# Performance work log

Measured on AMD Instinct MI355X. Metric: run time of the kernel, lower is better.

## Reference

```python
import jax, jax.numpy as jnp
import numpy as np

DEPTH = 13                 # tree depth -> N = 2**DEPTH - 1 reaches (heap layout, outlet = node 0)
N = 2 ** DEPTH - 1         # 8191 reaches
T = 2048                   # timesteps


def setup_inputs() -> dict:
    key = jax.random.key(0)
    ks = jax.random.split(key, 8)
    u = lambda k, shape, lo, hi: jax.random.uniform(k, shape, minval=lo, maxval=hi, dtype=jnp.float32)
    return {
        "lateral_inflows": u(ks[0], (T, N), 0.0, 2.0),     # m^3/s lateral inflow per reach
        "manning_n":       u(ks[1], (N,), 0.025, 0.06),    # Manning roughness
        "lengths":         u(ks[2], (N,), 1000.0, 5000.0), # reach length [m]
        "slopes":          u(ks[3], (N,), 1e-4, 1e-2),     # bed slope (>= 1e-4 as in source)
        "width_coefs":     u(ks[4], (N,), 3.0, 10.0),      # w = wc * Q**we  (power-law geometry)
        "width_exps":      u(ks[5], (N,), 0.4, 0.6),
        "depth_coefs":     u(ks[6], (N,), 0.2, 0.5),       # h = dc * Q**de
        "depth_exps":      u(ks[7], (N,), 0.3, 0.45),
        "dt": 3600,                                        # routing timestep [s]
    }


def _mc_outflow(I_new, I_old, O_old, n, L, S, wc, we, dc, de, dt):
    """Variable-parameter Muskingum-Cunge update for one vector of reaches."""
    Qr = jnp.maximum(0.5 * (I_new + O_old), 1e-3)          # reference discharge
    h = dc * Qr ** de                                       # hydraulic depth
    w = wc * Qr ** we                                       # top width
    v = h ** (2.0 / 3.0) * jnp.sqrt(S) / n                  # Manning velocity
    c = jnp.maximum((5.0 / 3.0) * v, 1e-3)                  # kinematic celerity
    K = L / c                                               # travel time
    X = jnp.clip(0.5 * (1.0 - Qr / (w * S * c * L)), 0.0, 0.5)
    den = 2.0 * K * (1.0 - X) + dt
    C1 = (dt - 2.0 * K * X) / den
    C2 = (dt + 2.0 * K * X) / den
    C3 = (2.0 * K * (1.0 - X) - dt) / den
    return jnp.maximum(C1 * I_new + C2 * I_old + C3 * O_old, 0.0)


def reference(lateral_inflows, manning_n, lengths, slopes, width_coefs, width_exps,
              depth_coefs, depth_exps, dt):
    dtf = jnp.float32(dt)
    Np = lateral_inflows.shape[1]
    params = (manning_n, lengths, slopes, width_coefs, width_exps, depth_coefs, depth_exps)

    def step(carry, lat_t):
        I_old, O_old = carry                                # [N] prev inflow / outflow
        Q = jnp.zeros(Np, dtype=lat_t.dtype)                # new outflows this timestep
        I_all = jnp.zeros(Np, dtype=lat_t.dtype)
        # process levels leaves -> root (reverse topological order over the DAG)
        for l in range(DEPTH - 1, -1, -1):
            s, e = 2 ** l - 1, 2 ** (l + 1) - 1             # nodes of level l
            if l == DEPTH - 1:
                up = jnp.float32(0.0)                        # headwater reaches
            else:
                cs, ce = 2 ** (l + 1) - 1, 2 ** (l + 2) - 1  # children = level l+1
                up = Q[cs:ce:2] + Q[cs + 1:ce:2]             # sum of 2 upstream discharges
            I_new = lat_t[s:e] + up
            O_new = _mc_outflow(I_new, I_old[s:e], O_old[s:e],
                                *(p[s:e] for p in params), dtf)
            Q = Q.at[s:e].set(O_new)
            I_all = I_all.at[s:e].set(I_new)
        return (I_all, Q), Q[0]                              # outlet = root (index 0)

    init = (jnp.zeros(Np, jnp.float32), jnp.zeros(Np, jnp.float32))
    _, outlet_Q = jax.lax.scan(step, init, lateral_inflows)
    return outlet_Q                                          # [T]
```

## Files before the change

### kernel.cpp

```cpp
#include <hip/hip_runtime.h>


#define NN 8191
#define TT 2048
#define FBATCH 32
#define NBLK 39
#define BTHREADS 256

#define FLAGS_FOFF 16773120ull
#define REQ_BYTES  67106816ull
#define FLAG_STRIDE 16

#if __has_builtin(__builtin_amdgcn_exp2f)
__device__ __forceinline__ float fexp2(float x) { return __builtin_amdgcn_exp2f(x); }
#else
__device__ __forceinline__ float fexp2(float x) { return exp2f(x); }
#endif
#if __has_builtin(__builtin_amdgcn_logf)
__device__ __forceinline__ float flog2(float x) { return __builtin_amdgcn_logf(x); }
#else
__device__ __forceinline__ float flog2(float x) { return log2f(x); }
#endif
#if __has_builtin(__builtin_amdgcn_rcpf)
__device__ __forceinline__ float frcp(float x) { return __builtin_amdgcn_rcpf(x); }
#else
__device__ __forceinline__ float frcp(float x) { return 1.0f / x; }
#endif

__constant__ int g_level[NBLK] = {
    12,12,12,12,12,12,12,12,12,12,12,12,12,12,12,12,
    11,11,11,11,11,11,11,11,
    10,10,10,10,
    9,9,
    8,7,6,5,4,3,2,1,0};
__constant__ int g_cnt[NBLK] = {
    256,256,256,256,256,256,256,256,256,256,256,256,256,256,256,256,
    256,256,256,256,256,256,256,256,
    256,256,256,256,
    256,256,
    256,128,64,32,16,8,4,2,1};
__constant__ int g_first[13] = {38,37,36,35,34,33,32,31,30,28,24,16,0};
__constant__ unsigned long long g_off[13] = {
    16773120ull, 16769024ull, 16760832ull, 16744448ull, 16711680ull,
    16646144ull, 16515072ull, 16252928ull, 15728640ull, 14680064ull,
    12582912ull, 8388608ull, 0ull};

__device__ __forceinline__ void waitflags(const unsigned int* fa, const unsigned int* fb,
                                          unsigned int target)
{
    while (true) {
        unsigned int a = __hip_atomic_load(fa, __ATOMIC_RELAXED, __HIP_MEMORY_SCOPE_AGENT);
        unsigned int b = fb ? __hip_atomic_load(fb, __ATOMIC_RELAXED, __HIP_MEMORY_SCOPE_AGENT)
                            : a;
        if (a >= target && b >= target) break;
        __builtin_amdgcn_s_sleep(1);
    }
    __builtin_amdgcn_sched_barrier(0);
    asm volatile("" ::: "memory");
}

__global__ void zero_flags(unsigned int* flags)
{
    for (int i = threadIdx.x; i < NBLK * 4 * FLAG_STRIDE; i += 256) flags[i] = 0;
}

__global__ __launch_bounds__(BTHREADS, 1)
void pipe_kernel(const float* __restrict__ lat,
                 const float* __restrict__ nman,
                 const float* __restrict__ len,
                 const float* __restrict__ slp,
                 const float* __restrict__ wcf,
                 const float* __restrict__ wex,
                 const float* __restrict__ dcf,
                 const float* __restrict__ dex,
                 const int*   __restrict__ dtp,
                 float*       __restrict__ out,
                 float*       __restrict__ ws)
{
    const int bid = blockIdx.x;
    const int tid = threadIdx.x;
    const int lvl = g_level[bid];
    const int cnt = g_cnt[bid];
    const int W   = tid >> 6;
    const int wn  = cnt - W * 64;
    if (wn <= 0) return;

    const bool active = (tid < cnt);
    const int B = bid - g_first[lvl];
    const int m = B * 256 + (active ? tid : 0);
    const int node = ((1 << lvl) - 1) + m;
    const int wbase = B * 256 + W * 64;

    unsigned int* flags = (unsigned int*)(ws + FLAGS_FOFF);
    unsigned int* myflag = flags + ((size_t)bid * 4 + W) * FLAG_STRIDE;

    const bool haschild = (lvl < 12);
    const unsigned int* fa = nullptr;
    const unsigned int* fb = nullptr;
    if (haschild) {
        const int Fp = g_first[lvl + 1];
        const int nw = wn < 64 ? wn : 64;
        const int p0 = (2 * wbase) >> 6;
        const int p1 = (2 * wbase + 2 * nw - 1) >> 6;
        fa = flags + ((size_t)(Fp + (p0 >> 2)) * 4 + (p0 & 3)) * FLAG_STRIDE;
        fb = (p1 != p0)
           ? flags + ((size_t)(Fp + (p1 >> 2)) * 4 + (p1 & 3)) * FLAG_STRIDE
           : nullptr;
    }

    const int myW = 1 << lvl;
    const int childW = 1 << (lvl + 1);
    float* myBuf = ws + g_off[lvl];
    const unsigned long long* childBuf =
        haschild ? (const unsigned long long*)(ws + g_off[lvl + 1]) : nullptr;

    const float dtf = (float)dtp[0];

    float em, tkc, ex, k1;
    float Iold = 0.0f, Oold = 0.0f;
    {
        float n = nman[node], L = len[node], S = slp[node];
        float wc = wcf[node], we = wex[node], dc = dcf[node], de = dex[node];
        float dc23 = fexp2(0.6666667f * flog2(dc));
        float cc = 1.6666667f * dc23 * sqrtf(S) * frcp(n);
        float e23 = 0.6666667f * de;
        em  = -e23;
        tkc = 2.0f * L * frcp(cc);
        ex  = 1.0f - we - e23;
        k1  = 0.5f * frcp(S * L * wc * cc);
    }

    float laA[FBATCH], laB[FBATCH];
    unsigned long long cvA[FBATCH], cvB[FBATCH];

#define LATBURST(dst, tb)                                                      \
    if (active) {                                                              \
        _Pragma("unroll")                                                      \
        for (int k = 0; k < FBATCH; ++k) {                                     \
            const float* lp_ = lat + (size_t)((tb) + k) * NN + node;           \
            asm volatile("global_load_dword %0, %1, off"                       \
                         : "=v"(dst[k]) : "v"(lp_));                           \
        }                                                                      \
    }

#define CHILDBURST(dst, tb)                                                    \
    if (haschild && active) {                                                  \
        _Pragma("unroll")                                                      \
        for (int k = 0; k < FBATCH; ++k) {                                     \
            const unsigned long long* cp_ =                                    \
                childBuf + (((size_t)((tb) + k) * childW) >> 1) + m;           \
            asm volatile("global_load_dwordx2 %0, %1, off sc0 sc1"             \
                         : "=v"(dst[k]) : "v"(cp_));                           \
        }                                                                      \
    }

#define CHAIN(laC, cvC, tb)                                                    \
    if (active) {                                                              \
        _Pragma("unroll")                                                      \
        for (int k = 0; k < FBATCH; ++k) {                                     \
            float ch_ = 0.0f;                                                  \
            if (haschild) {                                                    \
                float c0_ = __uint_as_float((unsigned int)(cvC[k] & 0xffffffffull)); \
                float c1_ = __uint_as_float((unsigned int)(cvC[k] >> 32));     \
                ch_ = c0_ + c1_;                                               \
            }                                                                  \
            float Inew = laC[k] + ch_;                                         \
            float Qr = fmaxf(0.5f * (Inew + Oold), 1e-3f);                     \
            float lg = flog2(Qr);                                              \
            float twoK = tkc * fexp2(em * lg);                                 \
            float X = fmaxf(0.5f - k1 * fexp2(ex * lg), 0.0f);                 \
            float A = twoK * X;                                                \
            float Bv = twoK - A;                                               \
            float r = frcp(Bv + dtf);                                          \
            float num = dtf * (Inew + Iold - Oold) + A * (Iold - Inew) + Bv * Oold; \
            float O = fmaxf(num * r, 0.0f);                                    \
            Iold = Inew; Oold = O;                                             \
            if (lvl > 0)                                                       \
                __hip_atomic_store(myBuf + (size_t)((tb) + k) * myW + m, O,    \
                                   __ATOMIC_RELAXED, __HIP_MEMORY_SCOPE_AGENT);\
            else                                                               \
                out[(tb) + k] = O;                                             \
        }                                                                      \
    }

#define PHASE(laC, cvC, laN, cvN, T0)                                          \
    do {                                                                       \
        const int t1_ = (T0) + FBATCH;                                         \
        if (t1_ < TT) {                                                        \
            LATBURST(laN, t1_);                                                \
            if (haschild) waitflags(fa, fb, (unsigned int)(t1_ + FBATCH));     \
            CHILDBURST(cvN, t1_);                                              \
        }                                                                      \
        CHAIN(laC, cvC, (T0));                                                 \
        asm volatile("s_waitcnt vmcnt(0)" ::: "memory");                       \
        __builtin_amdgcn_sched_barrier(0);                                     \
        if (lvl > 0 && (tid & 63) == 0)                                        \
            __hip_atomic_store(myflag, (unsigned int)((T0) + FBATCH),          \
                               __ATOMIC_RELAXED, __HIP_MEMORY_SCOPE_AGENT);    \
    } while (0)

    LATBURST(laA, 0);
    if (haschild) waitflags(fa, fb, (unsigned int)FBATCH);
    CHILDBURST(cvA, 0);
    asm volatile("s_waitcnt vmcnt(0)" ::: "memory");
    __builtin_amdgcn_sched_barrier(0);

    for (int t0 = 0; t0 < TT; t0 += 2 * FBATCH) {
        PHASE(laA, cvA, laB, cvB, t0);
        PHASE(laB, cvB, laA, cvA, t0 + FBATCH);
    }
#undef LATBURST
#undef CHILDBURST
#undef CHAIN
#undef PHASE
}

#define NTHREADS 1024
__device__ __forceinline__ float mc_update_fb(float Inew, float Iold, float Oold,
                                              float em, float tkc, float ex, float k1,
                                              float dtf)
{
    float Qr = fmaxf(0.5f * (Inew + Oold), 1e-3f);
    float lg = flog2(Qr);
    float twoK = tkc * fexp2(em * lg);
    float X = fmaxf(0.5f - k1 * fexp2(ex * lg), 0.0f);
    float A = twoK * X;
    float B = twoK - A;
    float r = frcp(B + dtf);
    float C1 = (dtf - A) * r;
    float C2 = (dtf + A) * r;
    float C3 = (B - dtf) * r;
    return fmaxf(C1 * Inew + C2 * Iold + C3 * Oold, 0.0f);
}

__global__ __launch_bounds__(NTHREADS)
void route_kernel(const float* __restrict__ lat,
                  const float* __restrict__ nman,
                  const float* __restrict__ len,
                  const float* __restrict__ slp,
                  const float* __restrict__ wcf,
                  const float* __restrict__ wex,
                  const float* __restrict__ dcf,
                  const float* __restrict__ dex,
                  const int*   __restrict__ dtp,
                  float*       __restrict__ out)
{
    __shared__ float Osh[NN];
    const int tid = threadIdx.x;
    const float dtf = (float)dtp[0];

    int nodes[8];
    nodes[0] = 4095 + tid;
    nodes[1] = 5119 + tid;
    nodes[2] = 6143 + tid;
    nodes[3] = 7167 + tid;
    nodes[4] = 2047 + tid;
    nodes[5] = 3071 + tid;
    nodes[6] = 1023 + tid;
    nodes[7] = (tid < 1023) ? tid : 0;

    float em[8], tkc[8], ex[8], k1[8];
    float Ireg[8], Oreg[8];
#pragma unroll
    for (int k = 0; k < 8; ++k) {
        int i = nodes[k];
        float n = nman[i], L = len[i], S = slp[i];
        float wc = wcf[i], we = wex[i], dc = dcf[i], de = dex[i];
        float dc23 = fexp2(0.6666667f * flog2(dc));
        float cc = 1.6666667f * dc23 * sqrtf(S) * frcp(n);
        float e23 = 0.6666667f * de;
        em[k]  = -e23;
        tkc[k] = 2.0f * L * frcp(cc);
        ex[k]  = 1.0f - we - e23;
        k1[k]  = 0.5f * frcp(S * L * wc * cc);
        Ireg[k] = 0.0f; Oreg[k] = 0.0f;
    }
    for (int i = tid; i < NN; i += NTHREADS) Osh[i] = 0.0f;
    __syncthreads();

    for (int t = 0; t < TT; ++t) {
        const float* __restrict__ latt = lat + (size_t)t * NN;
#pragma unroll
        for (int k = 0; k < 4; ++k) {
            int i = nodes[k];
            float Inew = latt[i];
            float O = mc_update_fb(Inew, Ireg[k], Oreg[k], em[k], tkc[k], ex[k], k1[k], dtf);
            Ireg[k] = Inew; Oreg[k] = O; Osh[i] = O;
        }
        __syncthreads();
#pragma unroll
        for (int k = 4; k < 6; ++k) {
            int i = nodes[k];
            float Inew = latt[i] + Osh[2 * i + 1] + Osh[2 * i + 2];
            float O = mc_update_fb(Inew, Ireg[k], Oreg[k], em[k], tkc[k], ex[k], k1[k], dtf);
            Ireg[k] = Inew; Oreg[k] = O; Osh[i] = O;
        }
        __syncthreads();
        {
            int i = nodes[6];
            float Inew = latt[i] + Osh[2 * i + 1] + Osh[2 * i + 2];
            float O = mc_update_fb(Inew, Ireg[6], Oreg[6], em[6], tkc[6], ex[6], k1[6], dtf);
            Ireg[6] = Inew; Oreg[6] = O; Osh[i] = O;
        }
        __syncthreads();
        for (int l = 9; l >= 0; --l) {
            int s = (1 << l) - 1;
            int e = (1 << (l + 1)) - 1;
            if (tid >= s && tid < e) {
                int i = tid;
                float Inew = latt[i] + Osh[2 * i + 1] + Osh[2 * i + 2];
                float O = mc_update_fb(Inew, Ireg[7], Oreg[7], em[7], tkc[7], ex[7], k1[7], dtf);
                Ireg[7] = Inew; Oreg[7] = O; Osh[i] = O;
            }
            __syncthreads();
        }
        if (tid == 0) out[t] = Oreg[7];
    }
}

extern "C" void kernel_launch(void* const* d_in, const int* in_sizes, int n_in,
                              void* d_out, int out_size, void* d_ws, size_t ws_size,
                              hipStream_t stream) {
    const float* lat  = (const float*)d_in[0];
    const float* nman = (const float*)d_in[1];
    const float* len  = (const float*)d_in[2];
    const float* slp  = (const float*)d_in[3];
    const float* wcf  = (const float*)d_in[4];
    const float* wex  = (const float*)d_in[5];
    const float* dcf  = (const float*)d_in[6];
    const float* dex  = (const float*)d_in[7];
    const int*   dtp  = (const int*)d_in[8];
    float* out = (float*)d_out;

    if (ws_size >= REQ_BYTES) {
        float* ws = (float*)d_ws;
        unsigned int* flags = (unsigned int*)(ws + FLAGS_FOFF);
        zero_flags<<<dim3(1), dim3(256), 0, stream>>>(flags);
        pipe_kernel<<<dim3(NBLK), dim3(BTHREADS), 0, stream>>>(
            lat, nman, len, slp, wcf, wex, dcf, dex, dtp, out, ws);
    } else {
        route_kernel<<<dim3(1), dim3(NTHREADS), 0, stream>>>(
            lat, nman, len, slp, wcf, wex, dcf, dex, dtp, out);
    }
}
```

Baseline: 455.6 us.

## Overlap flag polling and prefetch bursts with the recurrence chain; simplify MC algebra

Splits the per-batch serial Muskingum-Cunge chain into three segments and places the lateral prefetch plus a non-blocking flag load between them. The flag value is checked later, and the child-discharge burst is issued mid-chain, so flag-polling latency is hidden behind compute instead of stalling before it. It also rewrites the coefficient algebra, folding k1 and tkc into precomputed constants and recombining the numerator to shorten the dependent arithmetic per step. The risks are the extra vmcnt(0) wait inside FLAGCHECK, which also waits on the lateral loads mid-chain, and small floating-point differences from the reordered algebra.

```diff
diff --git a/kernel.cpp b/kernel.cpp
--- a/kernel.cpp
+++ b/kernel.cpp
@@ -116,7 +116,7 @@
 
     const float dtf = (float)dtp[0];
 
-    float em, tkc, ex, k1;
+    float em, eme, tkc, p1c, p2c;
     float Iold = 0.0f, Oold = 0.0f;
     {
         float n = nman[node], L = len[node], S = slp[node];
@@ -125,13 +125,16 @@
         float cc = 1.6666667f * dc23 * sqrtf(S) * frcp(n);
         float e23 = 0.6666667f * de;
         em  = -e23;
+        eme = 1.0f - we - 2.0f * e23;
         tkc = 2.0f * L * frcp(cc);
-        ex  = 1.0f - we - e23;
-        k1  = 0.5f * frcp(S * L * wc * cc);
+        float k1 = 0.5f * frcp(S * L * wc * cc);
+        p1c = 0.5f * tkc;
+        p2c = k1 * tkc;
     }
 
     float laA[FBATCH], laB[FBATCH];
     unsigned long long cvA[FBATCH], cvB[FBATCH];
+    unsigned int fva = 0xFFFFFFFFu, fvb = 0xFFFFFFFFu;
 
 #define LATBURST(dst, tb)                                                      \
     if (active) {                                                              \
@@ -154,10 +157,27 @@
         }                                                                      \
     }
 
-#define CHAIN(laC, cvC, tb)                                                    \
+#define FLAGLOAD()                                                             \
+    if (haschild) {                                                            \
+        asm volatile("global_load_dword %0, %1, off sc0 sc1"                   \
+                     : "=v"(fva) : "v"(fa));                                   \
+        if (fb)                                                                \
+            asm volatile("global_load_dword %0, %1, off sc0 sc1"               \
+                         : "=v"(fvb) : "v"(fb));                               \
+    }
+
+#define FLAGCHECK(TGT)                                                         \
+    if (haschild) {                                                            \
+        asm volatile("s_waitcnt vmcnt(0)"                                      \
+                     : "+v"(fva), "+v"(fvb) :: "memory");                      \
+        unsigned int tgt_ = (unsigned int)(TGT);                               \
+        if (fva < tgt_ || fvb < tgt_) waitflags(fa, fb, tgt_);                 \
+    }
+
+#define UPDS(laC, cvC, T0, K0, K1)                                             \
     if (active) {                                                              \
         _Pragma("unroll")                                                      \
-        for (int k = 0; k < FBATCH; ++k) {                                     \
+        for (int k = (K0); k < (K1); ++k) {                                    \
             float ch_ = 0.0f;                                                  \
             if (haschild) {                                                    \
                 float c0_ = __uint_as_float((unsigned int)(cvC[k] & 0xffffffffull)); \
@@ -167,31 +187,41 @@
             float Inew = laC[k] + ch_;                                         \
             float Qr = fmaxf(0.5f * (Inew + Oold), 1e-3f);                     \
             float lg = flog2(Qr);                                              \
-            float twoK = tkc * fexp2(em * lg);                                 \
-            float X = fmaxf(0.5f - k1 * fexp2(ex * lg), 0.0f);                 \
-            float A = twoK * X;                                                \
-            float Bv = twoK - A;                                               \
-            float r = frcp(Bv + dtf);                                          \
-            float num = dtf * (Inew + Iold - Oold) + A * (Iold - Inew) + Bv * Oold; \
+            float E1  = fexp2(em * lg);                                        \
+            float E12 = fexp2(eme * lg);                                       \
+            float twoK = tkc * E1;                                             \
+            float A = fmaxf(p1c * E1 - p2c * E12, 0.0f);                       \
+            float den = (twoK + dtf) - A;                                      \
+            float r = frcp(den);                                               \
+            float s1 = Inew + Iold - Oold;                                     \
+            float s2 = s1 - 2.0f * Inew;                                       \
+            float pre = twoK * Oold + dtf * s1;                                \
+            float num = pre + A * s2;                                          \
             float O = fmaxf(num * r, 0.0f);                                    \
             Iold = Inew; Oold = O;                                             \
             if (lvl > 0)                                                       \
-                __hip_atomic_store(myBuf + (size_t)((tb) + k) * myW + m, O,    \
+                __hip_atomic_store(myBuf + (size_t)((T0) + k) * myW + m, O,    \
                                    __ATOMIC_RELAXED, __HIP_MEMORY_SCOPE_AGENT);\
             else                                                               \
-                out[(tb) + k] = O;                                             \
+                out[(T0) + k] = O;                                             \
         }                                                                      \
     }
 
 #define PHASE(laC, cvC, laN, cvN, T0)                                          \
     do {                                                                       \
         const int t1_ = (T0) + FBATCH;                                         \
-        if (t1_ < TT) {                                                        \
-            LATBURST(laN, t1_);                                                \
-            if (haschild) waitflags(fa, fb, (unsigned int)(t1_ + FBATCH));     \
+        const bool hn_ = (t1_ < TT);                                           \
+        fva = 0xFFFFFFFFu; fvb = 0xFFFFFFFFu;                                  \
+        UPDS(laC, cvC, (T0), 0, 10);                                           \
+        if (hn_) { LATBURST(laN, t1_); FLAGLOAD(); }                           \
+        UPDS(laC, cvC, (T0), 10, 20);                                          \
+        if (hn_) {                                                             \
+            FLAGCHECK(t1_ + FBATCH);                                           \
+            __builtin_amdgcn_sched_barrier(0);                                 \
             CHILDBURST(cvN, t1_);                                              \
+            __builtin_amdgcn_sched_barrier(0);                                 \
         }                                                                      \
-        CHAIN(laC, cvC, (T0));                                                 \
+        UPDS(laC, cvC, (T0), 20, FBATCH);                                      \
         asm volatile("s_waitcnt vmcnt(0)" ::: "memory");                       \
         __builtin_amdgcn_sched_barrier(0);                                     \
         if (lvl > 0 && (tid & 63) == 0)                                        \
@@ -211,7 +241,9 @@
     }
 #undef LATBURST
 #undef CHILDBURST
-#undef CHAIN
+#undef FLAGLOAD
+#undef FLAGCHECK
+#undef UPDS
 #undef PHASE
 }
 
```

New measurement: 442.5 us. -2.9%, faster.
